# Optimization experiments

Measured on AMD Instinct MI355X. Metric: run time of the kernel, lower is better.

Reference implementation:

```python
import jax, jax.numpy as jnp
import numpy as np

B, S, V, E, H, T = 32, 512, 30522, 768, 768, 9


def lstm_layer(x, Wih, Whh, bih, bhh):
    # x: [B, S, In]; torch gate order i, f, g, o
    b = x.shape[0]
    h0 = jnp.zeros((b, Whh.shape[1]), x.dtype)
    def step(carry, xt):
        h, c = carry
        g = xt @ Wih.T + h @ Whh.T + bih + bhh
        i, f, gg, o = jnp.split(g, 4, axis=-1)
        c = jax.nn.sigmoid(f) * c + jax.nn.sigmoid(i) * jnp.tanh(gg)
        h = jax.nn.sigmoid(o) * jnp.tanh(c)
        return (h, c), h
    _, hs = jax.lax.scan(step, (h0, h0), jnp.swapaxes(x, 0, 1))
    return jnp.swapaxes(hs, 0, 1)


def crf_nll_token_mean(emissions, tags, mask, start_t, end_t, trans):
    # emissions [B,S,T] (log-softmaxed), tags [B,S] int, mask [B,S] bool
    maskf = mask.astype(emissions.dtype)
    em_at_tag = jnp.take_along_axis(emissions, tags[..., None], axis=2)[..., 0]  # [B,S]
    num = start_t[tags[:, 0]] + em_at_tag[:, 0]
    num = num + jnp.sum((trans[tags[:, :-1], tags[:, 1:]] + em_at_tag[:, 1:]) * maskf[:, 1:], axis=1)
    last_idx = jnp.sum(mask, axis=1) - 1
    last_tags = jnp.take_along_axis(tags, last_idx[:, None], axis=1)[:, 0]
    num = num + end_t[last_tags]
    # log-partition via masked forward recursion
    def step(score, inp):
        em_t, m_t = inp
        nxt = jax.nn.logsumexp(score[:, :, None] + trans[None], axis=1) + em_t
        return jnp.where(m_t[:, None], nxt, score), None
    score0 = start_t[None] + emissions[:, 0]
    ems = jnp.swapaxes(emissions[:, 1:], 0, 1)   # [S-1,B,T]
    ms = jnp.swapaxes(mask[:, 1:], 0, 1)         # [S-1,B]
    score, _ = jax.lax.scan(step, score0, (ems, ms))
    denom = jax.nn.logsumexp(score + end_t[None], axis=1)
    llh = num - denom
    return -jnp.sum(llh) / jnp.sum(maskf)


def crf_decode(emissions, mask, start_t, end_t, trans):
    b, s, t = emissions.shape
    ident = jnp.broadcast_to(jnp.arange(t)[None], (b, t))
    def step(score, inp):
        em_t, m_t = inp
        broad = score[:, :, None] + trans[None]          # [B, prev, next]
        nxt = jnp.max(broad, axis=1) + em_t
        idx = jnp.argmax(broad, axis=1)
        score = jnp.where(m_t[:, None], nxt, score)
        idx = jnp.where(m_t[:, None], idx, ident)        # identity on padded steps
        return score, idx
    score0 = start_t[None] + emissions[:, 0]
    ems = jnp.swapaxes(emissions[:, 1:], 0, 1)
    ms = jnp.swapaxes(mask[:, 1:], 0, 1)
    score, hist = jax.lax.scan(step, score0, (ems, ms))  # hist [S-1,B,T]
    best = jnp.argmax(score + end_t[None], axis=1)       # [B]
    def back(tag, idx_t):
        prev = jnp.take_along_axis(idx_t, tag[:, None], axis=1)[:, 0]
        return prev, prev
    _, prevs = jax.lax.scan(back, best, hist, reverse=True)  # [S-1,B]
    tags = jnp.concatenate([prevs, best[None]], axis=0)      # [S,B]
    return jnp.swapaxes(tags, 0, 1)


def setup_inputs() -> dict:
    key = jax.random.key(0)
    ks = jax.random.split(key, 16)
    input_ids = jax.random.randint(ks[0], (B, S), 0, V, dtype=jnp.int64)
    labels = jax.random.randint(ks[1], (B, S), 0, T, dtype=jnp.int64)
    lengths = jax.random.randint(ks[2], (B,), S // 2, S + 1)
    attention_mask = (jnp.arange(S)[None] < lengths[:, None]).astype(jnp.int32)
    def nrm(k, shape, scale):
        return scale * jax.random.normal(k, shape, dtype=jnp.float32)
    sc = 1.0 / np.sqrt(H)
    return {
        'input_ids': input_ids,
        'attention_mask': attention_mask,
        'labels': labels,
        'emb': nrm(ks[3], (V, E), 0.02),
        'Wih0': nrm(ks[4], (4 * H, E), sc), 'Whh0': nrm(ks[5], (4 * H, H), sc),
        'bih0': nrm(ks[6], (4 * H,), sc), 'bhh0': nrm(ks[7], (4 * H,), sc),
        'Wih1': nrm(ks[8], (4 * H, H), sc), 'Whh1': nrm(ks[9], (4 * H, H), sc),
        'bih1': nrm(ks[10], (4 * H,), sc), 'bhh1': nrm(ks[11], (4 * H,), sc),
        'Wout': nrm(ks[12], (T, H), sc), 'bout': jnp.zeros((T,), jnp.float32),
        'start_t': nrm(ks[13], (T,), 0.1),
        'end_t': nrm(ks[14], (T,), 0.1),
        'trans': nrm(ks[15], (T, T), 0.1),
    }


def reference(input_ids, attention_mask, labels, emb, Wih0, Whh0, bih0, bhh0,
              Wih1, Whh1, bih1, bhh1, Wout, bout, start_t, end_t, trans):
    mask = attention_mask.astype(bool)
    x = emb[input_ids]                                   # [B,S,E]
    h = lstm_layer(x, Wih0, Whh0, bih0, bhh0)
    h = lstm_layer(h, Wih1, Whh1, bih1, bhh1)
    logits = h @ Wout.T + bout                           # [B,S,T]
    logp = jax.nn.log_softmax(logits, axis=2)
    loss = crf_nll_token_mean(logp, labels, mask, start_t, end_t, trans)
    preds = crf_decode(logp, mask, start_t, end_t, trans) * attention_mask.astype(jnp.int64)
    return loss, preds
```

## Files before the change

### kernel.cpp

```cpp
#include <hip/hip_runtime.h>
#include <math.h>

#define BB 32
#define SS 512
#define VV 30522
#define EE 768
#define HH 768
#define TT 9
#define G4 (4*HH)
#define NBLK 96

__global__ void embed_kernel(const int* __restrict__ ids,
                             const float* __restrict__ emb,
                             float* __restrict__ x) {
    const int row = blockIdx.x;
    const int e4  = threadIdx.x;
    const int id  = ids[row];
    *(float4*)&x[(size_t)row * EE + e4 * 4] =
        *(const float4*)&emb[(size_t)id * EE + e4 * 4];
}

__global__ __launch_bounds__(256) void gemm_simple(
    const float* __restrict__ A, const float* __restrict__ W,
    const float* __restrict__ bias1, const float* __restrict__ bias2,
    float* __restrict__ C, int M, int N, int K) {
    __shared__ float As[16][65];
    __shared__ float Ws[16][65];
    const int tid = threadIdx.x;
    const int tx = tid & 15, ty = tid >> 4;
    const int m0 = blockIdx.y * 64, n0 = blockIdx.x * 64;
    float acc[4][4];
    #pragma unroll
    for (int i = 0; i < 4; ++i)
        #pragma unroll
        for (int j = 0; j < 4; ++j) acc[i][j] = 0.f;

    for (int k0 = 0; k0 < K; k0 += 16) {
        #pragma unroll
        for (int i = 0; i < 4; ++i) {
            int r = ty + i * 16;
            As[tx][r] = A[(size_t)(m0 + r) * K + k0 + tx];
            Ws[tx][r] = W[(size_t)(n0 + r) * K + k0 + tx];
        }
        __syncthreads();
        #pragma unroll
        for (int kk = 0; kk < 16; ++kk) {
            float ar[4], br[4];
            #pragma unroll
            for (int i = 0; i < 4; ++i) ar[i] = As[kk][ty * 4 + i];
            #pragma unroll
            for (int j = 0; j < 4; ++j) br[j] = Ws[kk][tx * 4 + j];
            #pragma unroll
            for (int i = 0; i < 4; ++i)
                #pragma unroll
                for (int j = 0; j < 4; ++j) acc[i][j] += ar[i] * br[j];
        }
        __syncthreads();
    }
    #pragma unroll
    for (int i = 0; i < 4; ++i) {
        int r = m0 + ty * 4 + i;
        #pragma unroll
        for (int j = 0; j < 4; ++j) {
            int c = n0 + tx * 4 + j;
            C[(size_t)r * N + c] = acc[i][j] + bias1[c] + bias2[c];
        }
    }
}

__global__ __launch_bounds__(256) void pack_whh(const float* __restrict__ Whh,
                                                float* __restrict__ wpk) {
    const int id = blockIdx.x * 256 + threadIdx.x;
    const int u = id / 768;
    const int k = id - u * 768;
    float4 o;
    o.x = Whh[(size_t)(0 * 768 + u) * 768 + k];
    o.y = Whh[(size_t)(1 * 768 + u) * 768 + k];
    o.z = Whh[(size_t)(2 * 768 + u) * 768 + k];
    o.w = Whh[(size_t)(3 * 768 + u) * 768 + k];
    *(float4*)&wpk[(size_t)id * 4] = o;
}

__global__ void init_bars(unsigned* __restrict__ bar) {
    if (threadIdx.x < 2) bar[threadIdx.x] = 0u;
}

__global__ __launch_bounds__(256) void lstm_layer_persist(
    const float* __restrict__ xW,
    const float* __restrict__ wpk,
    float* __restrict__ h_out,
    float* __restrict__ hTa,
    float* __restrict__ hTb,
    unsigned* __restrict__ bar) {
    extern __shared__ float smem[];
    float4* wlds = (float4*)smem;
    float*  hs   = smem + 24576;
    const int tid = threadIdx.x;
    const int ul = tid & 7;
    const int b  = tid >> 3;
    const int u  = blockIdx.x * 8 + ul;

    const float4* wp4 = (const float4*)wpk;
    for (int idx = tid; idx < 6144; idx += 256) {
        int k  = idx >> 3;
        int uu = idx & 7;
        wlds[idx] = wp4[(size_t)(blockIdx.x * 8 + uu) * 768 + k];
    }
    __syncthreads();

    float c = 0.f;
    for (int t = 0; t < SS; ++t) {
        const size_t row = (size_t)b * SS + t;
        float gi = xW[row * G4 + 0 * HH + u];
        float gf = xW[row * G4 + 1 * HH + u];
        float gg = xW[row * G4 + 2 * HH + u];
        float go = xW[row * G4 + 3 * HH + u];

        if (t > 0) {
            const float* hin = (t & 1) ? hTb : hTa;
            float a0 = 0.f, a1 = 0.f, a2 = 0.f, a3 = 0.f;
            for (int k0 = 0; k0 < 768; k0 += 256) {
                __syncthreads();
                const float4* src = (const float4*)(hin + k0 * 32);
                float4* dst = (float4*)hs;
                #pragma unroll
                for (int r = 0; r < 8; ++r) dst[r * 256 + tid] = src[r * 256 + tid];
                __syncthreads();
                const float4* wp = wlds + k0 * 8 + ul;
                #pragma unroll 8
                for (int kk = 0; kk < 256; ++kk) {
                    float hv = hs[kk * 32 + b];
                    float4 wv = wp[kk * 8];
                    a0 += wv.x * hv; a1 += wv.y * hv;
                    a2 += wv.z * hv; a3 += wv.w * hv;
                }
            }
            gi += a0; gf += a1; gg += a2; go += a3;
        }

        float si = 1.f / (1.f + expf(-gi));
        float sf = 1.f / (1.f + expf(-gf));
        float so = 1.f / (1.f + expf(-go));
        float tg = tanhf(gg);
        c = sf * c + si * tg;
        float h = so * tanhf(c);
        h_out[row * HH + u] = h;
        float* hout = (t & 1) ? hTa : hTb;
        hout[u * 32 + b] = h;

        if (t < SS - 1) {
            __syncthreads();
            if (tid == 0) {
                __builtin_amdgcn_fence(__ATOMIC_RELEASE, "agent");
                atomicAdd(bar, 1u);
                const unsigned target = (unsigned)(t + 1) * NBLK;
                while (__hip_atomic_load(bar, __ATOMIC_RELAXED,
                                         __HIP_MEMORY_SCOPE_AGENT) < target)
                    __builtin_amdgcn_s_sleep(1);
                __builtin_amdgcn_fence(__ATOMIC_ACQUIRE, "agent");
            }
            __syncthreads();
        }
    }
}

__global__ __launch_bounds__(256) void logits_kernel(
    const float* __restrict__ h, const float* __restrict__ Wout,
    const float* __restrict__ bout, float* __restrict__ logp) {
    const int row = blockIdx.x * 256 + threadIdx.x;
    const float* hr = &h[(size_t)row * HH];
    float lg[TT];
    for (int tt = 0; tt < TT; ++tt) {
        const float* wr = &Wout[tt * HH];
        float ps = 0.f;
        for (int k = 0; k < HH; ++k) ps += hr[k] * wr[k];
        lg[tt] = ps + bout[tt];
    }
    float mx = lg[0];
    for (int tt = 1; tt < TT; ++tt) mx = fmaxf(mx, lg[tt]);
    float sm = 0.f;
    for (int tt = 0; tt < TT; ++tt) sm += expf(lg[tt] - mx);
    float lse = mx + logf(sm);
    for (int tt = 0; tt < TT; ++tt) logp[(size_t)row * TT + tt] = lg[tt] - lse;
}

#define NEG_INF_F -3.0e38f
__global__ __launch_bounds__(64) void crf_forward(
    const float* __restrict__ logp, const int* __restrict__ labels,
    const int* __restrict__ mask, const float* __restrict__ start_t,
    const float* __restrict__ end_t, const float* __restrict__ trans,
    float* __restrict__ bstats) {
    const int b = blockIdx.x;
    const int lane = threadIdx.x;
    const int j = lane < TT ? lane : TT - 1;
    const float* em = logp + (size_t)b * SS * TT;
    const int* mk = mask + b * SS;
    const int* lb = labels + b * SS;
    float tr[TT];
    #pragma unroll
    for (int i = 0; i < TT; ++i) tr[i] = trans[i * TT + j];
    float sc = start_t[j] + em[j];

    for (int t = 1; t < SS; ++t) {
        const int m = mk[t];
        const float e = em[t * TT + j];
        float v[TT];
        #pragma unroll
        for (int i = 0; i < TT; ++i) v[i] = __shfl(sc, i) + tr[i];
        float mx = v[0];
        #pragma unroll
        for (int i = 1; i < TT; ++i) mx = fmaxf(mx, v[i]);
        float smv = 0.f;
        #pragma unroll
        for (int i = 0; i < TT; ++i) smv += expf(v[i] - mx);
        float nxt = mx + logf(smv) + e;
        sc = m ? nxt : sc;
    }
    float fin = sc + end_t[j];
    float fv[TT];
    #pragma unroll
    for (int i = 0; i < TT; ++i) fv[i] = __shfl(fin, i);
    float mx = fv[0];
    #pragma unroll
    for (int i = 1; i < TT; ++i) mx = fmaxf(mx, fv[i]);
    float smv = 0.f;
    #pragma unroll
    for (int i = 0; i < TT; ++i) smv += expf(fv[i] - mx);
    float denom = mx + logf(smv);
    float np = 0.f; int ic = 0;
    for (int t = lane; t < SS; t += 64) {
        int m = mk[t];
        ic += m;
        if (t > 0 && m) {
            int tg = lb[t], tp = lb[t - 1];
            np += trans[tp * TT + tg] + em[t * TT + tg];
        }
    }
    for (int off = 32; off; off >>= 1) {
        np += __shfl_down(np, off);
        ic += __shfl_down(ic, off);
    }
    if (lane == 0) {
        int tg0 = lb[0];
        np += start_t[tg0] + em[tg0];
        int tgl = lb[ic - 1];
        np += end_t[tgl];
        bstats[b * 3 + 0] = np;
        bstats[b * 3 + 1] = denom;
        bstats[b * 3 + 2] = (float)ic;
    }
}

__global__ __launch_bounds__(64) void crf_decode(
    const float* __restrict__ logp, const int* __restrict__ mask,
    const float* __restrict__ start_t, const float* __restrict__ end_t,
    const float* __restrict__ trans, float* __restrict__ preds) {
    __shared__ unsigned char bp[SS][TT];
    if (threadIdx.x != 0) return;
    const int b = blockIdx.x;
    const float* em = logp + (size_t)b * SS * TT;
    const int* mk = mask + b * SS;
    float sc[TT], nx[TT];
    for (int jj = 0; jj < TT; ++jj) sc[jj] = start_t[jj] + em[jj];

    for (int t = 1; t < SS; ++t) {
        const int m = mk[t];
        for (int jj = 0; jj < TT; ++jj) {
            float bmv = NEG_INF_F; int bi = 0;
            for (int i = 0; i < TT; ++i) {
                float v = sc[i] + trans[i * TT + jj];
                if (v > bmv) { bmv = v; bi = i; }
            }
            nx[jj] = bmv + em[t * TT + jj];
            bp[t][jj] = (unsigned char)(m ? bi : jj);
        }
        if (m) for (int jj = 0; jj < TT; ++jj) sc[jj] = nx[jj];
    }
    float bm = NEG_INF_F; int best = 0;
    for (int jj = 0; jj < TT; ++jj) {
        float v = sc[jj] + end_t[jj];
        if (v > bm) { bm = v; best = jj; }
    }
    int tag = best;
    preds[b * SS + (SS - 1)] = (float)(mk[SS - 1] ? tag : 0);
    for (int t = SS - 1; t >= 1; --t) {
        tag = bp[t][tag];
        preds[b * SS + t - 1] = (float)(mk[t - 1] ? tag : 0);
    }
}

__global__ void loss_kernel(const float* __restrict__ bstats,
                            float* __restrict__ out) {
    const int lane = threadIdx.x;
    float nd = 0.f, c = 0.f;
    if (lane < 32) {
        nd = bstats[lane * 3] - bstats[lane * 3 + 1];
        c  = bstats[lane * 3 + 2];
    }
    for (int off = 32; off; off >>= 1) {
        nd += __shfl_down(nd, off);
        c  += __shfl_down(c, off);
    }
    if (lane == 0) out[0] = -nd / c;
}

extern "C" void kernel_launch(void* const* d_in, const int* in_sizes, int n_in,
                              void* d_out, int out_size, void* d_ws, size_t ws_size,
                              hipStream_t stream) {
    const int*   ids   = (const int*)d_in[0];
    const int*   amask = (const int*)d_in[1];
    const int*   labels= (const int*)d_in[2];
    const float* emb   = (const float*)d_in[3];
    const float* Wih0  = (const float*)d_in[4];
    const float* Whh0  = (const float*)d_in[5];
    const float* bih0  = (const float*)d_in[6];
    const float* bhh0  = (const float*)d_in[7];
    const float* Wih1  = (const float*)d_in[8];
    const float* Whh1  = (const float*)d_in[9];
    const float* bih1  = (const float*)d_in[10];
    const float* bhh1  = (const float*)d_in[11];
    const float* Wout  = (const float*)d_in[12];
    const float* boutp = (const float*)d_in[13];
    const float* st    = (const float*)d_in[14];
    const float* et    = (const float*)d_in[15];
    const float* trp   = (const float*)d_in[16];

    float* ws     = (float*)d_ws;
    float* slab   = ws;
    float* xW     = slab + 12582912;
    float* hTa    = xW + 50331648;
    float* hTb    = hTa + 24576;
    float* wpk    = hTb + 24576;
    float* cb     = wpk + 2359296;
    float* logp   = cb + 24576;
    float* bstats = logp + 147456;
    unsigned* bar = (unsigned*)cb;
    float* out    = (float*)d_out;

    static bool attr_done = false;
    if (!attr_done) {
        hipFuncSetAttribute((const void*)lstm_layer_persist,
                            hipFuncAttributeMaxDynamicSharedMemorySize,
                            131072);
        attr_done = true;
    }

    dim3 ggrid(G4 / 64, (BB * SS) / 64);

    init_bars<<<1, 64, 0, stream>>>(bar);

    embed_kernel<<<BB * SS, EE / 4, 0, stream>>>(ids, emb, slab);
    gemm_simple<<<ggrid, 256, 0, stream>>>(slab, Wih0, bih0, bhh0, xW,
                                           BB * SS, G4, EE);
    pack_whh<<<(HH * HH) / 256, 256, 0, stream>>>(Whh0, wpk);
    lstm_layer_persist<<<NBLK, 256, 131072, stream>>>(xW, wpk, slab,
                                                      hTa, hTb, bar + 0);

    gemm_simple<<<ggrid, 256, 0, stream>>>(slab, Wih1, bih1, bhh1, xW,
                                           BB * SS, G4, HH);
    pack_whh<<<(HH * HH) / 256, 256, 0, stream>>>(Whh1, wpk);
    lstm_layer_persist<<<NBLK, 256, 131072, stream>>>(xW, wpk, slab,
                                                      hTa, hTb, bar + 1);

    logits_kernel<<<(BB * SS) / 256, 256, 0, stream>>>(slab, Wout, boutp, logp);

    crf_forward<<<32, 64, 0, stream>>>(logp, labels, amask, st, et, trp, bstats);
    crf_decode<<<32, 64, 0, stream>>>(logp, amask, st, et, trp, out + 1);
    loss_kernel<<<1, 64, 0, stream>>>(bstats, out);
}
```

Before: 26.55 ms.

## Split LSTM recurrent matvec across gate warps reading h directly from global

Restructures the persistent LSTM step so each of four wavefronts computes one gate's recurrent dot product for 8 units times 32 batch entries, each thread accumulating 4 batch entries. h is read as float4 straight from the global transposed buffer rather than staged through shared memory in three chunks. Partial sums are combined through a small shared reduction buffer, and only the first wavefront applies the nonlinearities and writes h. This drops the separate Whh pack kernel by loading padded weight rows directly, removes per-chunk syncthreads, and cuts shared memory use. The trade-off is that three quarters of the threads sit idle during the gate math, and every thread now issues global/L2 reads of h on each step.

```diff
diff --git a/kernel.cpp b/kernel.cpp
--- a/kernel.cpp
+++ b/kernel.cpp
@@ -68,85 +68,109 @@
     }
 }
 
-__global__ __launch_bounds__(256) void pack_whh(const float* __restrict__ Whh,
-                                                float* __restrict__ wpk) {
-    const int id = blockIdx.x * 256 + threadIdx.x;
-    const int u = id / 768;
-    const int k = id - u * 768;
-    float4 o;
-    o.x = Whh[(size_t)(0 * 768 + u) * 768 + k];
-    o.y = Whh[(size_t)(1 * 768 + u) * 768 + k];
-    o.z = Whh[(size_t)(2 * 768 + u) * 768 + k];
-    o.w = Whh[(size_t)(3 * 768 + u) * 768 + k];
-    *(float4*)&wpk[(size_t)id * 4] = o;
-}
-
 __global__ void init_bars(unsigned* __restrict__ bar) {
     if (threadIdx.x < 2) bar[threadIdx.x] = 0u;
 }
 
 __global__ __launch_bounds__(256) void lstm_layer_persist(
     const float* __restrict__ xW,
-    const float* __restrict__ wpk,
+    const float* __restrict__ Whh,
     float* __restrict__ h_out,
     float* __restrict__ hTa,
     float* __restrict__ hTb,
     unsigned* __restrict__ bar) {
     extern __shared__ float smem[];
-    float4* wlds = (float4*)smem;
-    float*  hs   = smem + 24576;
-    const int tid = threadIdx.x;
-    const int ul = tid & 7;
-    const int b  = tid >> 3;
-    const int u  = blockIdx.x * 8 + ul;
-
-    const float4* wp4 = (const float4*)wpk;
+    float*  wlds = smem;
+    float4* red  = (float4*)(smem + 24704);
+    const int tid  = threadIdx.x;
+    const int lane = tid & 63;
+    const int g    = tid >> 6;
+    const int uloc = lane >> 3;
+    const int bq   = lane & 7;
+    const int u    = blockIdx.x * 8 + uloc;
+    const bool owner = (tid < 64);
+
     for (int idx = tid; idx < 6144; idx += 256) {
-        int k  = idx >> 3;
-        int uu = idx & 7;
-        wlds[idx] = wp4[(size_t)(blockIdx.x * 8 + uu) * 768 + k];
+        const int gg  = idx / 1536;
+        const int rem = idx - gg * 1536;
+        const int uu  = rem / 192;
+        const int k4  = rem - uu * 192;
+        *(float4*)&wlds[gg * 6176 + uu * 772 + k4 * 4] =
+            *(const float4*)&Whh[(size_t)(gg * 768 + blockIdx.x * 8 + uu) * 768
+                                 + k4 * 4];
     }
     __syncthreads();
 
-    float c = 0.f;
+    const float* wrow = wlds + g * 6176 + uloc * 772;
+    float cc[4] = {0.f, 0.f, 0.f, 0.f};
+
     for (int t = 0; t < SS; ++t) {
-        const size_t row = (size_t)b * SS + t;
-        float gi = xW[row * G4 + 0 * HH + u];
-        float gf = xW[row * G4 + 1 * HH + u];
-        float gg = xW[row * G4 + 2 * HH + u];
-        float go = xW[row * G4 + 3 * HH + u];
+        float xg[4][4];
+        if (owner) {
+            #pragma unroll
+            for (int j = 0; j < 4; ++j) {
+                const size_t row = (size_t)(bq * 4 + j) * SS + t;
+                #pragma unroll
+                for (int gg = 0; gg < 4; ++gg)
+                    xg[j][gg] = xW[row * G4 + gg * HH + u];
+            }
+        }
 
         if (t > 0) {
-            const float* hin = (t & 1) ? hTb : hTa;
-            float a0 = 0.f, a1 = 0.f, a2 = 0.f, a3 = 0.f;
-            for (int k0 = 0; k0 < 768; k0 += 256) {
-                __syncthreads();
-                const float4* src = (const float4*)(hin + k0 * 32);
-                float4* dst = (float4*)hs;
+            const float4* hp = (const float4*)((t & 1) ? hTb : hTa);
+            float4 s = {0.f, 0.f, 0.f, 0.f};
+            #pragma unroll 4
+            for (int k4 = 0; k4 < 192; ++k4) {
+                const float4 w4 = *(const float4*)&wrow[k4 * 4];
+                const float4 h0 = hp[(k4 * 4 + 0) * 8 + bq];
+                const float4 h1 = hp[(k4 * 4 + 1) * 8 + bq];
+                const float4 h2 = hp[(k4 * 4 + 2) * 8 + bq];
+                const float4 h3 = hp[(k4 * 4 + 3) * 8 + bq];
+                s.x += w4.x * h0.x; s.y += w4.x * h0.y; s.z += w4.x * h0.z; s.w += w4.x * h0.w;
+                s.x += w4.y * h1.x; s.y += w4.y * h1.y; s.z += w4.y * h1.z; s.w += w4.y * h1.w;
+                s.x += w4.z * h2.x; s.y += w4.z * h2.y; s.z += w4.z * h2.z; s.w += w4.z * h2.w;
+                s.x += w4.w * h3.x; s.y += w4.w * h3.y; s.z += w4.w * h3.z; s.w += w4.w * h3.w;
+            }
+            red[g * 64 + lane] = s;
+        }
+        __syncthreads();
+
+        if (owner) {
+            float si_[4], sf_[4], sk_[4], so_[4];
+            if (t > 0) {
+                const float4 s0 = red[0 * 64 + lane];
+                const float4 s1 = red[1 * 64 + lane];
+                const float4 s2 = red[2 * 64 + lane];
+                const float4 s3 = red[3 * 64 + lane];
+                si_[0]=s0.x; si_[1]=s0.y; si_[2]=s0.z; si_[3]=s0.w;
+                sf_[0]=s1.x; sf_[1]=s1.y; sf_[2]=s1.z; sf_[3]=s1.w;
+                sk_[0]=s2.x; sk_[1]=s2.y; sk_[2]=s2.z; sk_[3]=s2.w;
+                so_[0]=s3.x; so_[1]=s3.y; so_[2]=s3.z; so_[3]=s3.w;
+            } else {
                 #pragma unroll
-                for (int r = 0; r < 8; ++r) dst[r * 256 + tid] = src[r * 256 + tid];
-                __syncthreads();
-                const float4* wp = wlds + k0 * 8 + ul;
-                #pragma unroll 8
-                for (int kk = 0; kk < 256; ++kk) {
-                    float hv = hs[kk * 32 + b];
-                    float4 wv = wp[kk * 8];
-                    a0 += wv.x * hv; a1 += wv.y * hv;
-                    a2 += wv.z * hv; a3 += wv.w * hv;
-                }
-            }
-            gi += a0; gf += a1; gg += a2; go += a3;
-        }
-
-        float si = 1.f / (1.f + expf(-gi));
-        float sf = 1.f / (1.f + expf(-gf));
-        float so = 1.f / (1.f + expf(-go));
-        float tg = tanhf(gg);
-        c = sf * c + si * tg;
-        float h = so * tanhf(c);
-        h_out[row * HH + u] = h;
-        float* hout = (t & 1) ? hTa : hTb;
-        hout[u * 32 + b] = h;
+                for (int j = 0; j < 4; ++j)
+                    si_[j] = sf_[j] = sk_[j] = so_[j] = 0.f;
+            }
+            float* hTo = (t & 1) ? hTa : hTb;
+            float hvv[4];
+            #pragma unroll
+            for (int j = 0; j < 4; ++j) {
+                const float gi = si_[j] + xg[j][0];
+                const float gf = sf_[j] + xg[j][1];
+                const float gg = sk_[j] + xg[j][2];
+                const float go = so_[j] + xg[j][3];
+                const float sI = 1.f / (1.f + expf(-gi));
+                const float sF = 1.f / (1.f + expf(-gf));
+                const float sO = 1.f / (1.f + expf(-go));
+                const float tG = tanhf(gg);
+                cc[j] = sF * cc[j] + sI * tG;
+                const float h = sO * tanhf(cc[j]);
+                hvv[j] = h;
+                h_out[((size_t)(bq * 4 + j) * SS + t) * HH + u] = h;
+            }
+            *(float4*)&hTo[u * 32 + bq * 4] =
+                make_float4(hvv[0], hvv[1], hvv[2], hvv[3]);
+        }
 
         if (t < SS - 1) {
             __syncthreads();
@@ -336,12 +360,13 @@
     float* bstats = logp + 147456;
     unsigned* bar = (unsigned*)cb;
     float* out    = (float*)d_out;
+    (void)wpk;
 
     static bool attr_done = false;
     if (!attr_done) {
         hipFuncSetAttribute((const void*)lstm_layer_persist,
                             hipFuncAttributeMaxDynamicSharedMemorySize,
-                            131072);
+                            102912);
         attr_done = true;
     }
 
@@ -352,14 +377,12 @@
     embed_kernel<<<BB * SS, EE / 4, 0, stream>>>(ids, emb, slab);
     gemm_simple<<<ggrid, 256, 0, stream>>>(slab, Wih0, bih0, bhh0, xW,
                                            BB * SS, G4, EE);
-    pack_whh<<<(HH * HH) / 256, 256, 0, stream>>>(Whh0, wpk);
-    lstm_layer_persist<<<NBLK, 256, 131072, stream>>>(xW, wpk, slab,
+    lstm_layer_persist<<<NBLK, 256, 102912, stream>>>(xW, Whh0, slab,
                                                       hTa, hTb, bar + 0);
 
     gemm_simple<<<ggrid, 256, 0, stream>>>(slab, Wih1, bih1, bhh1, xW,
                                            BB * SS, G4, HH);
-    pack_whh<<<(HH * HH) / 256, 256, 0, stream>>>(Whh1, wpk);
-    lstm_layer_persist<<<NBLK, 256, 131072, stream>>>(xW, wpk, slab,
+    lstm_layer_persist<<<NBLK, 256, 102912, stream>>>(xW, Whh1, slab,
                                                       hTa, hTb, bar + 1);
 
     logits_kernel<<<(BB * SS) / 256, 256, 0, stream>>>(slab, Wout, boutp, logp);
```

After: 35.13 ms. 1.32x slower.

## Warp-specialize LSTM recurrence: one wave computes 4x4 tiles while others prefetch h

Applied to the files above, without the earlier changes.

The persistent LSTM kernel is restructured so the first 64 threads each compute a 4-batch by 4-gate register tile over the hidden dimension. The remaining 192 threads double-buffer the next chunk of the previous hidden state into LDS, overlapping that copy with the math. This raises arithmetic intensity per LDS load and hides global-to-LDS copies. In exchange only one wave does the FMAs, which may lower ALU utilization and lengthen the serial per-step critical path.

```diff
diff --git a/kernel.cpp b/kernel.cpp
--- a/kernel.cpp
+++ b/kernel.cpp
@@ -93,60 +93,95 @@
     float* __restrict__ hTb,
     unsigned* __restrict__ bar) {
     extern __shared__ float smem[];
-    float4* wlds = (float4*)smem;
-    float*  hs   = smem + 24576;
+    float4* wlds4 = (float4*)smem;
+    float*  hs    = smem + 24576;
     const int tid = threadIdx.x;
-    const int ul = tid & 7;
-    const int b  = tid >> 3;
-    const int u  = blockIdx.x * 8 + ul;
+    const int ul  = tid >> 3;
+    const int bq  = tid & 7;
+    const int u   = blockIdx.x * 8 + ul;
+    const bool owner = (tid < 64);
 
     const float4* wp4 = (const float4*)wpk;
     for (int idx = tid; idx < 6144; idx += 256) {
-        int k  = idx >> 3;
-        int uu = idx & 7;
-        wlds[idx] = wp4[(size_t)(blockIdx.x * 8 + uu) * 768 + k];
+        const int k  = idx >> 3;
+        const int uu = idx & 7;
+        wlds4[idx] = wp4[(size_t)(blockIdx.x * 8 + uu) * 768 + k];
     }
     __syncthreads();
 
-    float c = 0.f;
+    float cc[4] = {0.f, 0.f, 0.f, 0.f};
+
     for (int t = 0; t < SS; ++t) {
-        const size_t row = (size_t)b * SS + t;
-        float gi = xW[row * G4 + 0 * HH + u];
-        float gf = xW[row * G4 + 1 * HH + u];
-        float gg = xW[row * G4 + 2 * HH + u];
-        float go = xW[row * G4 + 3 * HH + u];
-
+        float xg[4][4];
+        if (owner) {
+            #pragma unroll
+            for (int j = 0; j < 4; ++j) {
+                const size_t row = (size_t)(bq * 4 + j) * SS + t;
+                #pragma unroll
+                for (int gg = 0; gg < 4; ++gg)
+                    xg[j][gg] = xW[row * G4 + gg * HH + u];
+            }
+        }
+
+        float4 aI = {0,0,0,0}, aF = {0,0,0,0}, aG = {0,0,0,0}, aO = {0,0,0,0};
         if (t > 0) {
-            const float* hin = (t & 1) ? hTb : hTa;
-            float a0 = 0.f, a1 = 0.f, a2 = 0.f, a3 = 0.f;
-            for (int k0 = 0; k0 < 768; k0 += 256) {
-                __syncthreads();
-                const float4* src = (const float4*)(hin + k0 * 32);
+            const float4* hp = (const float4*)((t & 1) ? hTb : hTa);
+
+            {
                 float4* dst = (float4*)hs;
                 #pragma unroll
-                for (int r = 0; r < 8; ++r) dst[r * 256 + tid] = src[r * 256 + tid];
+                for (int r = 0; r < 4; ++r) dst[r * 256 + tid] = hp[r * 256 + tid];
+            }
+            __syncthreads();
+
+            for (int c = 0; c < 6; ++c) {
+                if (tid >= 64 && c + 1 < 6) {
+                    const float4* src = hp + (size_t)(c + 1) * 1024;
+                    float4* dst = (float4*)(hs + ((c + 1) & 1) * 4096);
+                    for (int i = tid - 64; i < 1024; i += 192) dst[i] = src[i];
+                }
+                if (owner) {
+                    const float4* hb = (const float4*)(hs + (c & 1) * 4096);
+                    const float4* wb = wlds4 + c * 128 * 8;
+                    #pragma unroll 8
+                    for (int kk = 0; kk < 128; ++kk) {
+                        const float4 w4 = wb[kk * 8 + ul];
+                        const float4 hv = hb[kk * 8 + bq];
+                        aI.x += w4.x*hv.x; aI.y += w4.x*hv.y; aI.z += w4.x*hv.z; aI.w += w4.x*hv.w;
+                        aF.x += w4.y*hv.x; aF.y += w4.y*hv.y; aF.z += w4.y*hv.z; aF.w += w4.y*hv.w;
+                        aG.x += w4.z*hv.x; aG.y += w4.z*hv.y; aG.z += w4.z*hv.z; aG.w += w4.z*hv.w;
+                        aO.x += w4.w*hv.x; aO.y += w4.w*hv.y; aO.z += w4.w*hv.z; aO.w += w4.w*hv.w;
+                    }
+                }
                 __syncthreads();
-                const float4* wp = wlds + k0 * 8 + ul;
-                #pragma unroll 8
-                for (int kk = 0; kk < 256; ++kk) {
-                    float hv = hs[kk * 32 + b];
-                    float4 wv = wp[kk * 8];
-                    a0 += wv.x * hv; a1 += wv.y * hv;
-                    a2 += wv.z * hv; a3 += wv.w * hv;
-                }
-            }
-            gi += a0; gf += a1; gg += a2; go += a3;
-        }
-
-        float si = 1.f / (1.f + expf(-gi));
-        float sf = 1.f / (1.f + expf(-gf));
-        float so = 1.f / (1.f + expf(-go));
-        float tg = tanhf(gg);
-        c = sf * c + si * tg;
-        float h = so * tanhf(c);
-        h_out[row * HH + u] = h;
-        float* hout = (t & 1) ? hTa : hTb;
-        hout[u * 32 + b] = h;
+            }
+        }
+
+        if (owner) {
+            const float si_[4] = {aI.x, aI.y, aI.z, aI.w};
+            const float sf_[4] = {aF.x, aF.y, aF.z, aF.w};
+            const float sk_[4] = {aG.x, aG.y, aG.z, aG.w};
+            const float so_[4] = {aO.x, aO.y, aO.z, aO.w};
+            float* hTo = (t & 1) ? hTa : hTb;
+            float hvv[4];
+            #pragma unroll
+            for (int j = 0; j < 4; ++j) {
+                const float gi = si_[j] + xg[j][0];
+                const float gf = sf_[j] + xg[j][1];
+                const float gg = sk_[j] + xg[j][2];
+                const float go = so_[j] + xg[j][3];
+                const float sI = 1.f / (1.f + expf(-gi));
+                const float sF = 1.f / (1.f + expf(-gf));
+                const float sO = 1.f / (1.f + expf(-go));
+                const float tG = tanhf(gg);
+                cc[j] = sF * cc[j] + sI * tG;
+                const float h = sO * tanhf(cc[j]);
+                hvv[j] = h;
+                h_out[((size_t)(bq * 4 + j) * SS + t) * HH + u] = h;
+            }
+            *(float4*)&hTo[u * 32 + bq * 4] =
+                make_float4(hvv[0], hvv[1], hvv[2], hvv[3]);
+        }
 
         if (t < SS - 1) {
             __syncthreads();
```

Result: slower. 51.71 ms (+94.8%).

## Restructure persistent LSTM step: wave-per-unit with uniform weight loads

Applied to the files above, without the earlier changes.

The recurrent kernel moves from 256 threads with the per-block Whh slice held in LDS to 512 threads, one wave per hidden unit and lanes mapped to batch. The packed weights are now read from global memory with wave-uniform addresses (readfirstlane on the wave index), so the compiler can turn them into scalar loads. The h state is stored batch-major and copied once per step into padded LDS rows. This removes the chunked LDS staging loops and their repeated barriers. In exchange, upper half-waves compute duplicate results, and weights are re-fetched from cache on every timestep.

```diff
diff --git a/kernel.cpp b/kernel.cpp
--- a/kernel.cpp
+++ b/kernel.cpp
@@ -85,7 +85,7 @@
     if (threadIdx.x < 2) bar[threadIdx.x] = 0u;
 }
 
-__global__ __launch_bounds__(256) void lstm_layer_persist(
+__global__ __launch_bounds__(512) void lstm_layer_persist(
     const float* __restrict__ xW,
     const float* __restrict__ wpk,
     float* __restrict__ h_out,
@@ -93,60 +93,68 @@
     float* __restrict__ hTb,
     unsigned* __restrict__ bar) {
     extern __shared__ float smem[];
-    float4* wlds = (float4*)smem;
-    float*  hs   = smem + 24576;
     const int tid = threadIdx.x;
-    const int ul = tid & 7;
-    const int b  = tid >> 3;
-    const int u  = blockIdx.x * 8 + ul;
-
-    const float4* wp4 = (const float4*)wpk;
-    for (int idx = tid; idx < 6144; idx += 256) {
-        int k  = idx >> 3;
-        int uu = idx & 7;
-        wlds[idx] = wp4[(size_t)(blockIdx.x * 8 + uu) * 768 + k];
-    }
-    __syncthreads();
-
-    float c = 0.f;
+    const int w   = __builtin_amdgcn_readfirstlane(tid >> 6);
+    const int b   = tid & 31;
+    const int u   = blockIdx.x * 8 + w;
+    const bool owner = (tid & 63) < 32;
+
+    const float4* wp4 = (const float4*)wpk + (size_t)u * 768;
+    float cc = 0.f;
+
     for (int t = 0; t < SS; ++t) {
-        const size_t row = (size_t)b * SS + t;
-        float gi = xW[row * G4 + 0 * HH + u];
-        float gf = xW[row * G4 + 1 * HH + u];
-        float gg = xW[row * G4 + 2 * HH + u];
-        float go = xW[row * G4 + 3 * HH + u];
-
+        float xg0, xg1, xg2, xg3;
+        if (owner) {
+            const size_t row = (size_t)b * SS + t;
+            xg0 = xW[row * G4 + 0 * HH + u];
+            xg1 = xW[row * G4 + 1 * HH + u];
+            xg2 = xW[row * G4 + 2 * HH + u];
+            xg3 = xW[row * G4 + 3 * HH + u];
+        }
+
+        float a0 = 0.f, a1 = 0.f, a2 = 0.f, a3 = 0.f;
         if (t > 0) {
-            const float* hin = (t & 1) ? hTb : hTa;
-            float a0 = 0.f, a1 = 0.f, a2 = 0.f, a3 = 0.f;
-            for (int k0 = 0; k0 < 768; k0 += 256) {
-                __syncthreads();
-                const float4* src = (const float4*)(hin + k0 * 32);
-                float4* dst = (float4*)hs;
-                #pragma unroll
-                for (int r = 0; r < 8; ++r) dst[r * 256 + tid] = src[r * 256 + tid];
-                __syncthreads();
-                const float4* wp = wlds + k0 * 8 + ul;
-                #pragma unroll 8
-                for (int kk = 0; kk < 256; ++kk) {
-                    float hv = hs[kk * 32 + b];
-                    float4 wv = wp[kk * 8];
-                    a0 += wv.x * hv; a1 += wv.y * hv;
-                    a2 += wv.z * hv; a3 += wv.w * hv;
+            const float* hT_in = (t & 1) ? hTb : hTa;
+            {
+                const float4* src = (const float4*)hT_in;
+                for (int i = tid; i < 6144; i += 512) {
+                    const int bb = i / 192;
+                    const int u4 = i - bb * 192;
+                    *(float4*)&smem[bb * 772 + u4 * 4] = src[bb * 192 + u4];
                 }
             }
-            gi += a0; gf += a1; gg += a2; go += a3;
-        }
-
-        float si = 1.f / (1.f + expf(-gi));
-        float sf = 1.f / (1.f + expf(-gf));
-        float so = 1.f / (1.f + expf(-go));
-        float tg = tanhf(gg);
-        c = sf * c + si * tg;
-        float h = so * tanhf(c);
-        h_out[row * HH + u] = h;
-        float* hout = (t & 1) ? hTa : hTb;
-        hout[u * 32 + b] = h;
+            __syncthreads();
+
+            const float4* hrow = (const float4*)(smem + b * 772);
+            #pragma unroll 4
+            for (int k4 = 0; k4 < 192; ++k4) {
+                const float4 h4 = hrow[k4];
+                const float4 w0 = wp4[k4 * 4 + 0];
+                const float4 w1 = wp4[k4 * 4 + 1];
+                const float4 w2 = wp4[k4 * 4 + 2];
+                const float4 w3 = wp4[k4 * 4 + 3];
+                a0 += w0.x * h4.x; a1 += w0.y * h4.x; a2 += w0.z * h4.x; a3 += w0.w * h4.x;
+                a0 += w1.x * h4.y; a1 += w1.y * h4.y; a2 += w1.z * h4.y; a3 += w1.w * h4.y;
+                a0 += w2.x * h4.z; a1 += w2.y * h4.z; a2 += w2.z * h4.z; a3 += w2.w * h4.z;
+                a0 += w3.x * h4.w; a1 += w3.y * h4.w; a2 += w3.z * h4.w; a3 += w3.w * h4.w;
+            }
+        }
+
+        if (owner) {
+            const float gi = a0 + xg0;
+            const float gf = a1 + xg1;
+            const float gg = a2 + xg2;
+            const float go = a3 + xg3;
+            const float sI = 1.f / (1.f + expf(-gi));
+            const float sF = 1.f / (1.f + expf(-gf));
+            const float sO = 1.f / (1.f + expf(-go));
+            const float tG = tanhf(gg);
+            cc = sF * cc + sI * tG;
+            const float h = sO * tanhf(cc);
+            h_out[((size_t)b * SS + t) * HH + u] = h;
+            float* hTo = (t & 1) ? hTa : hTb;
+            hTo[b * 768 + u] = h;
+        }
 
         if (t < SS - 1) {
             __syncthreads();
@@ -353,14 +361,14 @@
     gemm_simple<<<ggrid, 256, 0, stream>>>(slab, Wih0, bih0, bhh0, xW,
                                            BB * SS, G4, EE);
     pack_whh<<<(HH * HH) / 256, 256, 0, stream>>>(Whh0, wpk);
-    lstm_layer_persist<<<NBLK, 256, 131072, stream>>>(xW, wpk, slab,
-                                                      hTa, hTb, bar + 0);
+    lstm_layer_persist<<<NBLK, 512, 98816, stream>>>(xW, wpk, slab,
+                                                     hTa, hTb, bar + 0);
 
     gemm_simple<<<ggrid, 256, 0, stream>>>(slab, Wih1, bih1, bhh1, xW,
                                            BB * SS, G4, HH);
     pack_whh<<<(HH * HH) / 256, 256, 0, stream>>>(Whh1, wpk);
-    lstm_layer_persist<<<NBLK, 256, 131072, stream>>>(xW, wpk, slab,
-                                                      hTa, hTb, bar + 1);
+    lstm_layer_persist<<<NBLK, 512, 98816, stream>>>(xW, wpk, slab,
+                                                     hTa, hTb, bar + 1);
 
     logits_kernel<<<(BB * SS) / 256, 256, 0, stream>>>(slab, Wout, boutp, logp);
 
```

New measurement: 29.84 ms. 12.4% more time.
